# Kernel optimization log

Hardware: AMD Instinct MI355X
Metric: run time of the kernel (lower is better)

Reference implementation:

```python
import jax, jax.numpy as jnp
import numpy as np

N_USERS = 100000
N_ITEMS = 200000
N = N_USERS + N_ITEMS
E = 1200000
D = 64
HEADS = 4
GCN_LAYERS = 2


def setup_inputs() -> dict:
    key = jax.random.key(0)
    ks = jax.random.split(key, 10)
    s = 1.0 / np.sqrt(D)
    return {
        "uEmbeds": jax.random.normal(ks[0], (N_USERS, D), jnp.float32) * s,
        "iEmbeds": jax.random.normal(ks[1], (N_ITEMS, D), jnp.float32) * s,
        "qTrans": jax.random.normal(ks[2], (D, D), jnp.float32) * s,
        "kTrans": jax.random.normal(ks[3], (D, D), jnp.float32) * s,
        "vTrans": jax.random.normal(ks[4], (D, D), jnp.float32) * s,
        "enc_vals": jax.random.uniform(ks[5], (E,), jnp.float32),
        "enc_rows": jax.random.randint(ks[6], (E,), 0, N, jnp.int32),
        "enc_cols": jax.random.randint(ks[7], (E,), 0, N, jnp.int32),
        "dec_rows": jax.random.randint(ks[8], (E,), 0, N, jnp.int32),
        "dec_cols": jax.random.randint(ks[9], (E,), 0, N, jnp.int32),
    }


def _gcn(vals, rows, cols, embeds):
    # spmm: out[r] += vals[e] * embeds[cols[e]]
    msg = vals[:, None] * embeds[cols]  # [E, D]
    return jax.ops.segment_sum(msg, rows, num_segments=N)


def _gt(rows, cols, qT, kT, vT, embeds):
    dh = D // HEADS
    rowE = embeds[rows]  # [E, D]
    colE = embeds[cols]  # [E, D]
    q = (rowE @ qT).reshape(-1, HEADS, dh)
    k = (colE @ kT).reshape(-1, HEADS, dh)
    v = (colE @ vT).reshape(-1, HEADS, dh)
    att = jnp.clip(jnp.einsum('ehd,ehd->eh', q, k), -10.0, 10.0)
    expAtt = jnp.exp(att)  # [E, H]
    attNorm = jax.ops.segment_sum(expAtt, rows, num_segments=N)[rows]
    a = expAtt / (attNorm + 1e-8)
    res = (a[..., None] * v).reshape(-1, D)  # [E, D]
    return jax.ops.segment_sum(res, rows, num_segments=N)


def reference(uEmbeds, iEmbeds, qTrans, kTrans, vTrans,
              enc_vals, enc_rows, enc_cols, dec_rows, dec_cols):
    embeds = jnp.concatenate([uEmbeds, iEmbeds], axis=0)  # [N, D]
    embedsLst = [embeds]
    for _ in range(GCN_LAYERS):
        embedsLst.append(_gcn(enc_vals, enc_rows, enc_cols, embedsLst[-1]))
    embedsLst.append(_gt(dec_rows, dec_cols, qTrans, kTrans, vTrans, embedsLst[-1]))
    out = embedsLst[0]
    for e in embedsLst[1:]:
        out = out + e
    return out[:N_USERS], out[N_USERS:]
```

## Files before the change

kernel.cpp:

```cpp
#include <hip/hip_runtime.h>
#include <math.h>

#define N_USERS 100000
#define NTOT    300000
#define NEDGE   1200000
#define DIM     64

#define NPBS    256
#define BROWS2  1172
#define CAPS    5376
#define SCHUNK  4096
#define NCH     ((NEDGE + SCHUNK - 1) / SCHUNK)
#define PAD5    1280

typedef unsigned short ushort_t;
typedef unsigned int uint_t;
typedef __attribute__((ext_vector_type(8))) short short8;
typedef __attribute__((ext_vector_type(4))) float f32x4;

__device__ __forceinline__ float bf2f(ushort_t u) {
    return __uint_as_float(((uint_t)u) << 16);
}
__device__ __forceinline__ ushort_t f2bf(float x) {
    uint_t b = __float_as_uint(x);
    b += 0x7FFFu + ((b >> 16) & 1u);
    return (ushort_t)(b >> 16);
}


__global__ __launch_bounds__(256) void convert_emb0(
    const float* __restrict__ uE, const float* __restrict__ iE,
    ushort_t* __restrict__ emb0b) {
    int i = blockIdx.x * 256 + threadIdx.x;
    if (i >= NTOT * 16) return;
    float4 x = (i < N_USERS * 16) ? reinterpret_cast<const float4*>(uE)[i]
                                  : reinterpret_cast<const float4*>(iE)[i - N_USERS * 16];
    ushort4 o;
    o.x = f2bf(x.x); o.y = f2bf(x.y); o.z = f2bf(x.z); o.w = f2bf(x.w);
    reinterpret_cast<ushort4*>(emb0b)[i] = o;
}

__global__ void bt_prep(const float* __restrict__ qT, const float* __restrict__ kT,
                        const float* __restrict__ vT, ushort_t* __restrict__ Bt) {
    int t = threadIdx.x;
    for (int idx = t; idx < 4096; idx += 256) {
        int k = idx >> 6, c = idx & 63;
        Bt[c * 64 + k]        = f2bf(qT[idx]);
        Bt[4096 + c * 64 + k] = f2bf(kT[idx]);
        Bt[8192 + c * 64 + k] = f2bf(vT[idx]);
    }
}

__global__ void init_gcur(int* __restrict__ gE, int* __restrict__ gD) {
    int t = threadIdx.x;
    gE[t] = t * CAPS;
    gD[t] = t * CAPS;
}

__global__ __launch_bounds__(256) void bucket_stage(
    const int* __restrict__ enc_rows, const int* __restrict__ enc_cols,
    const float* __restrict__ enc_vals, const int* __restrict__ dec_rows,
    const int* __restrict__ dec_cols, int* __restrict__ gcurE,
    int* __restrict__ gcurD, int2* __restrict__ stE, int* __restrict__ stD) {
    __shared__ int cnt[NPBS];
    __shared__ int base[NPBS];
    __shared__ int run[NPBS];
    int t = threadIdx.x;
    bool enc = blockIdx.x < NCH;
    int cb = (enc ? blockIdx.x : blockIdx.x - NCH) * SCHUNK;
    int ce = min(cb + SCHUNK, NEDGE);
    const int* rows = enc ? enc_rows : dec_rows;
    cnt[t] = 0; run[t] = 0;
    __syncthreads();
    for (int i = cb + t; i < ce; i += 256) atomicAdd(&cnt[rows[i] / BROWS2], 1);
    __syncthreads();
    base[t] = atomicAdd(enc ? &gcurE[t] : &gcurD[t], cnt[t]);
    __syncthreads();
    if (enc) {
        for (int i = cb + t; i < ce; i += 256) {
            int r = rows[i];
            int p = r / BROWS2;
            int off = atomicAdd(&run[p], 1);
            int2 v;
            v.x = ((r - p * BROWS2) << 19) | enc_cols[i];
            v.y = __float_as_int(enc_vals[i]);
            stE[base[p] + off] = v;
        }
    } else {
        for (int i = cb + t; i < ce; i += 256) {
            int r = rows[i];
            int p = r / BROWS2;
            int off = atomicAdd(&run[p], 1);
            stD[base[p] + off] = ((r - p * BROWS2) << 19) | dec_cols[i];
        }
    }
}

__global__ __launch_bounds__(256) void scanB(
    const int* __restrict__ gcurE, const int* __restrict__ gcurD,
    int* __restrict__ bbE, int* __restrict__ bbD,
    int* __restrict__ rsE, int* __restrict__ rsD) {
    __shared__ int sh[256];
    int t = threadIdx.x;
    int c = gcurE[t] - t * CAPS;
    sh[t] = c; __syncthreads();
    for (int off = 1; off < 256; off <<= 1) {
        int x = (t >= off) ? sh[t - off] : 0; __syncthreads();
        sh[t] += x; __syncthreads();
    }
    bbE[t] = sh[t] - c;
    __syncthreads();
    int cd = gcurD[t] - t * CAPS;
    sh[t] = cd; __syncthreads();
    for (int off = 1; off < 256; off <<= 1) {
        int x = (t >= off) ? sh[t - off] : 0; __syncthreads();
        sh[t] += x; __syncthreads();
    }
    bbD[t] = sh[t] - cd;
    if (t == 0) { rsE[NTOT] = NEDGE; rsD[NTOT] = NEDGE; }
}

__global__ __launch_bounds__(256) void sort_b(
    const int* __restrict__ gcurE, const int* __restrict__ gcurD,
    const int* __restrict__ bbE, const int* __restrict__ bbD,
    const int2* __restrict__ stE, const int* __restrict__ stD,
    int2* __restrict__ penc, int* __restrict__ pdec,
    int* __restrict__ rsE, int* __restrict__ rsD) {
    __shared__ int cnt[PAD5];
    __shared__ int rowst[PAD5];
    __shared__ int tsum[256];
    __shared__ int2 outb[CAPS];
    int t = threadIdx.x;
    bool enc = blockIdx.x < NPBS;
    int b = enc ? blockIdx.x : blockIdx.x - NPBS;
    int rowbase = b * BROWS2;
    int s = b * CAPS;
    int e = enc ? gcurE[b] : gcurD[b];
    int gbase = enc ? bbE[b] : bbD[b];
    int n = e - s;

    for (int i = t; i < PAD5; i += 256) cnt[i] = 0;
    __syncthreads();
    if (enc) {
        for (int i = s + t; i < e; i += 256)
            atomicAdd(&cnt[((uint_t)stE[i].x) >> 19], 1);
    } else {
        for (int i = s + t; i < e; i += 256)
            atomicAdd(&cnt[((uint_t)stD[i]) >> 19], 1);
    }
    __syncthreads();
    int b5 = t * 5, sum = 0;
#pragma unroll
    for (int k = 0; k < 5; ++k) { int c = cnt[b5 + k]; rowst[b5 + k] = sum; sum += c; }
    tsum[t] = sum; __syncthreads();
    for (int off = 1; off < 256; off <<= 1) {
        int x = (t >= off) ? tsum[t - off] : 0; __syncthreads();
        tsum[t] += x; __syncthreads();
    }
    int excl = tsum[t] - sum;
#pragma unroll
    for (int k = 0; k < 5; ++k) {
        rowst[b5 + k] += excl;
        cnt[b5 + k] = rowst[b5 + k];
    }
    __syncthreads();

    if (enc) {
        for (int i = s + t; i < e; i += 256) {
            int2 v = stE[i];
            int lr = ((uint_t)v.x) >> 19;
            int pos = atomicAdd(&cnt[lr], 1);
            outb[pos] = make_int2(v.x & 0x7FFFF, v.y);
        }
        __syncthreads();
        for (int i = t; i < n; i += 256) penc[gbase + i] = outb[i];
        int nrows = min(BROWS2, NTOT - rowbase);
        for (int j = t; j < nrows; j += 256) rsE[rowbase + j] = gbase + rowst[j];
    } else {
        int* ob = (int*)outb;
        for (int i = s + t; i < e; i += 256) {
            int v = stD[i];
            int pos = atomicAdd(&cnt[((uint_t)v) >> 19], 1);
            ob[pos] = v & 0x7FFFF;
        }
        __syncthreads();
        for (int i = t; i < n; i += 256) pdec[gbase + i] = ob[i];
        int nrows = min(BROWS2, NTOT - rowbase);
        for (int j = t; j < nrows; j += 256) rsD[rowbase + j] = gbase + rowst[j];
    }
}

__global__ __launch_bounds__(256) void gcn_gather1(
    const int* __restrict__ rsE, const int2* __restrict__ penc,
    const ushort_t* __restrict__ emb0b, ushort_t* __restrict__ emb1b) {
    int t = blockIdx.x * 256 + threadIdx.x;
    int row = t >> 4, l = t & 15;
    if (row >= NTOT) return;
    int s = rsE[row], e = rsE[row + 1];
    float4 acc = {0.f, 0.f, 0.f, 0.f};
    for (int j = s; j < e; ++j) {
        int2 cv = penc[j];
        float v = __int_as_float(cv.y);
        ushort4 xb = reinterpret_cast<const ushort4*>(emb0b + (size_t)cv.x * DIM)[l];
        acc.x += v * bf2f(xb.x); acc.y += v * bf2f(xb.y);
        acc.z += v * bf2f(xb.z); acc.w += v * bf2f(xb.w);
    }
    ushort4 o;
    o.x = f2bf(acc.x); o.y = f2bf(acc.y); o.z = f2bf(acc.z); o.w = f2bf(acc.w);
    reinterpret_cast<ushort4*>(emb1b)[(size_t)row * 16 + l] = o;
}

__global__ __launch_bounds__(256) void gcn_gather2(
    const int* __restrict__ rsE, const int2* __restrict__ penc,
    const ushort_t* __restrict__ emb1b, const float* __restrict__ uE,
    const float* __restrict__ iE, ushort_t* __restrict__ emb2b,
    float* __restrict__ out) {
    int t = blockIdx.x * 256 + threadIdx.x;
    int row = t >> 4, l = t & 15;
    if (row >= NTOT) return;
    int s = rsE[row], e = rsE[row + 1];
    float4 acc = {0.f, 0.f, 0.f, 0.f};
    for (int j = s; j < e; ++j) {
        int2 cv = penc[j];
        float v = __int_as_float(cv.y);
        ushort4 xb = reinterpret_cast<const ushort4*>(emb1b + (size_t)cv.x * DIM)[l];
        acc.x += v * bf2f(xb.x); acc.y += v * bf2f(xb.y);
        acc.z += v * bf2f(xb.z); acc.w += v * bf2f(xb.w);
    }
    const float* e0p = (row < N_USERS) ? uE + (size_t)row * DIM
                                       : iE + (size_t)(row - N_USERS) * DIM;
    float4 e0 = reinterpret_cast<const float4*>(e0p)[l];
    ushort4 e1b = reinterpret_cast<const ushort4*>(emb1b)[(size_t)row * 16 + l];
    ushort4 o2;
    o2.x = f2bf(acc.x); o2.y = f2bf(acc.y); o2.z = f2bf(acc.z); o2.w = f2bf(acc.w);
    reinterpret_cast<ushort4*>(emb2b)[(size_t)row * 16 + l] = o2;
    float4 o;
    o.x = e0.x + bf2f(e1b.x) + acc.x; o.y = e0.y + bf2f(e1b.y) + acc.y;
    o.z = e0.z + bf2f(e1b.z) + acc.z; o.w = e0.w + bf2f(e1b.w) + acc.w;
    reinterpret_cast<float4*>(out)[(size_t)row * 16 + l] = o;
}

__global__ __launch_bounds__(256) void qkv_mfma(
    const ushort_t* __restrict__ emb2b, const ushort_t* __restrict__ Bt,
    float* __restrict__ Q, ushort_t* __restrict__ KV) {
    int tid = threadIdx.x;
    int w = tid >> 6, lane = tid & 63;
    int lr = lane & 15, lh = lane >> 4;
    int R0 = blockIdx.x * 256 + w * 64;

    short8 a[4][2];
    short8 z8 = {0, 0, 0, 0, 0, 0, 0, 0};
#pragma unroll
    for (int m = 0; m < 4; ++m) {
        int row = R0 + m * 16 + lr;
        if (row < NTOT) {
            const ushort_t* ap = emb2b + (size_t)row * 64 + lh * 8;
            a[m][0] = *reinterpret_cast<const short8*>(ap);
            a[m][1] = *reinterpret_cast<const short8*>(ap + 32);
        } else {
            a[m][0] = z8; a[m][1] = z8;
        }
    }

#pragma unroll
    for (int n = 0; n < 4; ++n) {
        int col = n * 16 + lr;
        const ushort_t* bp = Bt + (size_t)col * 64 + lh * 8;
        short8 bq0 = *reinterpret_cast<const short8*>(bp);
        short8 bq1 = *reinterpret_cast<const short8*>(bp + 32);
        short8 bk0 = *reinterpret_cast<const short8*>(bp + 4096);
        short8 bk1 = *reinterpret_cast<const short8*>(bp + 4096 + 32);
        short8 bv0 = *reinterpret_cast<const short8*>(bp + 8192);
        short8 bv1 = *reinterpret_cast<const short8*>(bp + 8192 + 32);
#pragma unroll
        for (int m = 0; m < 4; ++m) {
            f32x4 aq = {0.f, 0.f, 0.f, 0.f};
            f32x4 ak = {0.f, 0.f, 0.f, 0.f};
            f32x4 av = {0.f, 0.f, 0.f, 0.f};
            aq = __builtin_amdgcn_mfma_f32_16x16x32_bf16(a[m][0], bq0, aq, 0, 0, 0);
            aq = __builtin_amdgcn_mfma_f32_16x16x32_bf16(a[m][1], bq1, aq, 0, 0, 0);
            ak = __builtin_amdgcn_mfma_f32_16x16x32_bf16(a[m][0], bk0, ak, 0, 0, 0);
            ak = __builtin_amdgcn_mfma_f32_16x16x32_bf16(a[m][1], bk1, ak, 0, 0, 0);
            av = __builtin_amdgcn_mfma_f32_16x16x32_bf16(a[m][0], bv0, av, 0, 0, 0);
            av = __builtin_amdgcn_mfma_f32_16x16x32_bf16(a[m][1], bv1, av, 0, 0, 0);
            int rbase = R0 + m * 16 + lh * 4;
#pragma unroll
            for (int r = 0; r < 4; ++r) {
                int srow = rbase + r;
                if (srow < NTOT) {
                    Q[(size_t)srow * 64 + col] = aq[r];
                    KV[(size_t)srow * 128 + col] = f2bf(ak[r]);
                    KV[(size_t)srow * 128 + 64 + col] = f2bf(av[r]);
                }
            }
        }
    }
}

__global__ __launch_bounds__(256) void gt_fused(
    const int* __restrict__ rsD, const int* __restrict__ pdec,
    const float* __restrict__ Q, const ushort_t* __restrict__ KV,
    float* __restrict__ out) {
    int t = blockIdx.x * 256 + threadIdx.x;
    int row = t >> 4, l = t & 15;
    if (row >= NTOT) return;
    int s = rsD[row], e = rsD[row + 1];
    float4 q = reinterpret_cast<const float4*>(Q)[(size_t)row * 16 + l];
    float norm = 0.f;
    float4 acc = {0.f, 0.f, 0.f, 0.f};
    for (int j = s; j < e; ++j) {
        int c = pdec[j];
        const ushort_t* kvrow = KV + (size_t)c * 128;
        ushort4 kb = reinterpret_cast<const ushort4*>(kvrow)[l];
        ushort4 vb = reinterpret_cast<const ushort4*>(kvrow)[16 + l];
        float p = q.x * bf2f(kb.x) + q.y * bf2f(kb.y)
                + q.z * bf2f(kb.z) + q.w * bf2f(kb.w);
        p += __shfl_xor(p, 1);
        p += __shfl_xor(p, 2);
        p = fminf(10.f, fmaxf(-10.f, p));
        float ex = __expf(p);
        norm += ex;
        acc.x += ex * bf2f(vb.x); acc.y += ex * bf2f(vb.y);
        acc.z += ex * bf2f(vb.z); acc.w += ex * bf2f(vb.w);
    }
    float inv = 1.f / (norm + 1e-8f);
    float4 o = reinterpret_cast<float4*>(out)[(size_t)row * 16 + l];
    o.x += acc.x * inv; o.y += acc.y * inv;
    o.z += acc.z * inv; o.w += acc.w * inv;
    reinterpret_cast<float4*>(out)[(size_t)row * 16 + l] = o;
}

extern "C" void kernel_launch(void* const* d_in, const int* in_sizes, int n_in,
                              void* d_out, int out_size, void* d_ws, size_t ws_size,
                              hipStream_t stream) {
    const float* uE       = (const float*)d_in[0];
    const float* iE       = (const float*)d_in[1];
    const float* qT       = (const float*)d_in[2];
    const float* kT       = (const float*)d_in[3];
    const float* vT       = (const float*)d_in[4];
    const float* enc_vals = (const float*)d_in[5];
    const int*   enc_rows = (const int*)d_in[6];
    const int*   enc_cols = (const int*)d_in[7];
    const int*   dec_rows = (const int*)d_in[8];
    const int*   dec_cols = (const int*)d_in[9];
    float* out = (float*)d_out;

    const size_t ND = (size_t)NTOT * DIM;
    ushort_t* emb0b = (ushort_t*)d_ws;
    ushort_t* emb1b = emb0b + ND;
    ushort_t* emb2b = emb1b + ND;
    ushort_t* KV    = emb2b + ND;
    ushort_t* Bt    = KV + 2 * ND;
    int*      rsE   = (int*)(Bt + 3 * 4096);
    int*      rsD   = rsE + NTOT + 1;
    int2*     penc  = (int2*)(rsD + NTOT + 1);
    int*      pdec  = (int*)(penc + NEDGE);
    int*      gcurE = pdec + NEDGE;
    int*      gcurD = gcurE + NPBS;
    int*      bbE   = gcurD + NPBS;
    int*      bbD   = bbE + NPBS;

    float*    Q     = (float*)emb0b;
    int2*     stE   = (int2*)KV;
    int*      stD   = (int*)(stE + (size_t)NPBS * CAPS);

    const int GB  = (NTOT * 16) / 256;
    const int QB  = (NTOT + 255) / 256;

    init_gcur<<<1, 256, 0, stream>>>(gcurE, gcurD);
    convert_emb0<<<GB, 256, 0, stream>>>(uE, iE, emb0b);
    bt_prep<<<1, 256, 0, stream>>>(qT, kT, vT, Bt);

    bucket_stage<<<2 * NCH, 256, 0, stream>>>(enc_rows, enc_cols, enc_vals,
                                              dec_rows, dec_cols, gcurE, gcurD, stE, stD);
    scanB<<<1, 256, 0, stream>>>(gcurE, gcurD, bbE, bbD, rsE, rsD);
    sort_b<<<2 * NPBS, 256, 0, stream>>>(gcurE, gcurD, bbE, bbD, stE, stD,
                                         penc, pdec, rsE, rsD);

    gcn_gather1<<<GB, 256, 0, stream>>>(rsE, penc, emb0b, emb1b);
    gcn_gather2<<<GB, 256, 0, stream>>>(rsE, penc, emb1b, uE, iE, emb2b, out);

    qkv_mfma<<<QB, 256, 0, stream>>>(emb2b, Bt, Q, KV);
    gt_fused<<<GB, 256, 0, stream>>>(rsD, pdec, Q, KV, out);
}
```

Before: 409.7 us.

## Use one wavefront per row with 8 edge slots in gather kernels

The three CSR gather kernels (two GCN layers and the attention aggregation) now assign a full 64-lane wavefront to each row instead of 16 lanes. The lanes split into 8 edge slots of 8 lanes, each lane loading 16-byte chunks, so several edges per row are in flight at once. Partial sums are combined with cross-slot shuffle reductions and only slot 0 writes. This aims to raise memory-level parallelism for rows averaging about 4 edges. The cost is many idle slots on short rows, extra shuffle reductions, and four times as many threads launched.

```diff
diff --git a/kernel.cpp b/kernel.cpp
--- a/kernel.cpp
+++ b/kernel.cpp
@@ -16,6 +16,7 @@
 typedef unsigned short ushort_t;
 typedef unsigned int uint_t;
 typedef __attribute__((ext_vector_type(8))) short short8;
+typedef __attribute__((ext_vector_type(8))) unsigned short ushort8;
 typedef __attribute__((ext_vector_type(4))) float f32x4;
 
 __device__ __forceinline__ float bf2f(ushort_t u) {
@@ -193,21 +194,30 @@
 __global__ __launch_bounds__(256) void gcn_gather1(
     const int* __restrict__ rsE, const int2* __restrict__ penc,
     const ushort_t* __restrict__ emb0b, ushort_t* __restrict__ emb1b) {
-    int t = blockIdx.x * 256 + threadIdx.x;
-    int row = t >> 4, l = t & 15;
+    int tid = blockIdx.x * 256 + threadIdx.x;
+    int row = tid >> 6;
     if (row >= NTOT) return;
+    int lane = threadIdx.x & 63;
+    int slot = lane >> 3, sub = lane & 7;
     int s = rsE[row], e = rsE[row + 1];
-    float4 acc = {0.f, 0.f, 0.f, 0.f};
-    for (int j = s; j < e; ++j) {
+    float acc[8] = {};
+    for (int j = s + slot; j < e; j += 8) {
         int2 cv = penc[j];
         float v = __int_as_float(cv.y);
-        ushort4 xb = reinterpret_cast<const ushort4*>(emb0b + (size_t)cv.x * DIM)[l];
-        acc.x += v * bf2f(xb.x); acc.y += v * bf2f(xb.y);
-        acc.z += v * bf2f(xb.z); acc.w += v * bf2f(xb.w);
-    }
-    ushort4 o;
-    o.x = f2bf(acc.x); o.y = f2bf(acc.y); o.z = f2bf(acc.z); o.w = f2bf(acc.w);
-    reinterpret_cast<ushort4*>(emb1b)[(size_t)row * 16 + l] = o;
+        ushort8 xb = *reinterpret_cast<const ushort8*>(emb0b + (size_t)cv.x * DIM + sub * 8);
+#pragma unroll
+        for (int k = 0; k < 8; ++k) acc[k] += v * bf2f(xb[k]);
+    }
+#pragma unroll
+    for (int m = 8; m <= 32; m <<= 1)
+#pragma unroll
+        for (int k = 0; k < 8; ++k) acc[k] += __shfl_xor(acc[k], m);
+    if (slot == 0) {
+        ushort8 o;
+#pragma unroll
+        for (int k = 0; k < 8; ++k) o[k] = f2bf(acc[k]);
+        *reinterpret_cast<ushort8*>(emb1b + (size_t)row * DIM + sub * 8) = o;
+    }
 }
 
 __global__ __launch_bounds__(256) void gcn_gather2(
@@ -215,29 +225,42 @@
     const ushort_t* __restrict__ emb1b, const float* __restrict__ uE,
     const float* __restrict__ iE, ushort_t* __restrict__ emb2b,
     float* __restrict__ out) {
-    int t = blockIdx.x * 256 + threadIdx.x;
-    int row = t >> 4, l = t & 15;
+    int tid = blockIdx.x * 256 + threadIdx.x;
+    int row = tid >> 6;
     if (row >= NTOT) return;
+    int lane = threadIdx.x & 63;
+    int slot = lane >> 3, sub = lane & 7;
     int s = rsE[row], e = rsE[row + 1];
-    float4 acc = {0.f, 0.f, 0.f, 0.f};
-    for (int j = s; j < e; ++j) {
+    float acc[8] = {};
+    for (int j = s + slot; j < e; j += 8) {
         int2 cv = penc[j];
         float v = __int_as_float(cv.y);
-        ushort4 xb = reinterpret_cast<const ushort4*>(emb1b + (size_t)cv.x * DIM)[l];
-        acc.x += v * bf2f(xb.x); acc.y += v * bf2f(xb.y);
-        acc.z += v * bf2f(xb.z); acc.w += v * bf2f(xb.w);
-    }
-    const float* e0p = (row < N_USERS) ? uE + (size_t)row * DIM
-                                       : iE + (size_t)(row - N_USERS) * DIM;
-    float4 e0 = reinterpret_cast<const float4*>(e0p)[l];
-    ushort4 e1b = reinterpret_cast<const ushort4*>(emb1b)[(size_t)row * 16 + l];
-    ushort4 o2;
-    o2.x = f2bf(acc.x); o2.y = f2bf(acc.y); o2.z = f2bf(acc.z); o2.w = f2bf(acc.w);
-    reinterpret_cast<ushort4*>(emb2b)[(size_t)row * 16 + l] = o2;
-    float4 o;
-    o.x = e0.x + bf2f(e1b.x) + acc.x; o.y = e0.y + bf2f(e1b.y) + acc.y;
-    o.z = e0.z + bf2f(e1b.z) + acc.z; o.w = e0.w + bf2f(e1b.w) + acc.w;
-    reinterpret_cast<float4*>(out)[(size_t)row * 16 + l] = o;
+        ushort8 xb = *reinterpret_cast<const ushort8*>(emb1b + (size_t)cv.x * DIM + sub * 8);
+#pragma unroll
+        for (int k = 0; k < 8; ++k) acc[k] += v * bf2f(xb[k]);
+    }
+#pragma unroll
+    for (int m = 8; m <= 32; m <<= 1)
+#pragma unroll
+        for (int k = 0; k < 8; ++k) acc[k] += __shfl_xor(acc[k], m);
+    if (slot == 0) {
+        ushort8 o2;
+#pragma unroll
+        for (int k = 0; k < 8; ++k) o2[k] = f2bf(acc[k]);
+        *reinterpret_cast<ushort8*>(emb2b + (size_t)row * DIM + sub * 8) = o2;
+        const float* e0p = (row < N_USERS) ? uE + (size_t)row * DIM
+                                           : iE + (size_t)(row - N_USERS) * DIM;
+        float4 e0a = reinterpret_cast<const float4*>(e0p)[sub * 2];
+        float4 e0b = reinterpret_cast<const float4*>(e0p)[sub * 2 + 1];
+        ushort8 e1 = *reinterpret_cast<const ushort8*>(emb1b + (size_t)row * DIM + sub * 8);
+        float4 oa, ob;
+        oa.x = e0a.x + bf2f(e1[0]) + acc[0]; oa.y = e0a.y + bf2f(e1[1]) + acc[1];
+        oa.z = e0a.z + bf2f(e1[2]) + acc[2]; oa.w = e0a.w + bf2f(e1[3]) + acc[3];
+        ob.x = e0b.x + bf2f(e1[4]) + acc[4]; ob.y = e0b.y + bf2f(e1[5]) + acc[5];
+        ob.z = e0b.z + bf2f(e1[6]) + acc[6]; ob.w = e0b.w + bf2f(e1[7]) + acc[7];
+        reinterpret_cast<float4*>(out + (size_t)row * DIM)[sub * 2] = oa;
+        reinterpret_cast<float4*>(out + (size_t)row * DIM)[sub * 2 + 1] = ob;
+    }
 }
 
 __global__ __launch_bounds__(256) void qkv_mfma(
@@ -301,33 +324,53 @@
     const int* __restrict__ rsD, const int* __restrict__ pdec,
     const float* __restrict__ Q, const ushort_t* __restrict__ KV,
     float* __restrict__ out) {
-    int t = blockIdx.x * 256 + threadIdx.x;
-    int row = t >> 4, l = t & 15;
+    int tid = blockIdx.x * 256 + threadIdx.x;
+    int row = tid >> 6;
     if (row >= NTOT) return;
+    int lane = threadIdx.x & 63;
+    int slot = lane >> 3, sub = lane & 7;
     int s = rsD[row], e = rsD[row + 1];
-    float4 q = reinterpret_cast<const float4*>(Q)[(size_t)row * 16 + l];
+    float qv[8];
+    {
+        float4 qa = reinterpret_cast<const float4*>(Q + (size_t)row * DIM)[sub * 2];
+        float4 qb = reinterpret_cast<const float4*>(Q + (size_t)row * DIM)[sub * 2 + 1];
+        qv[0] = qa.x; qv[1] = qa.y; qv[2] = qa.z; qv[3] = qa.w;
+        qv[4] = qb.x; qv[5] = qb.y; qv[6] = qb.z; qv[7] = qb.w;
+    }
     float norm = 0.f;
-    float4 acc = {0.f, 0.f, 0.f, 0.f};
-    for (int j = s; j < e; ++j) {
+    float acc[8] = {};
+    for (int j = s + slot; j < e; j += 8) {
         int c = pdec[j];
         const ushort_t* kvrow = KV + (size_t)c * 128;
-        ushort4 kb = reinterpret_cast<const ushort4*>(kvrow)[l];
-        ushort4 vb = reinterpret_cast<const ushort4*>(kvrow)[16 + l];
-        float p = q.x * bf2f(kb.x) + q.y * bf2f(kb.y)
-                + q.z * bf2f(kb.z) + q.w * bf2f(kb.w);
+        ushort8 kb = *reinterpret_cast<const ushort8*>(kvrow + sub * 8);
+        ushort8 vb = *reinterpret_cast<const ushort8*>(kvrow + 64 + sub * 8);
+        float p = 0.f;
+#pragma unroll
+        for (int k = 0; k < 8; ++k) p += qv[k] * bf2f(kb[k]);
         p += __shfl_xor(p, 1);
-        p += __shfl_xor(p, 2);
         p = fminf(10.f, fmaxf(-10.f, p));
         float ex = __expf(p);
         norm += ex;
-        acc.x += ex * bf2f(vb.x); acc.y += ex * bf2f(vb.y);
-        acc.z += ex * bf2f(vb.z); acc.w += ex * bf2f(vb.w);
-    }
-    float inv = 1.f / (norm + 1e-8f);
-    float4 o = reinterpret_cast<float4*>(out)[(size_t)row * 16 + l];
-    o.x += acc.x * inv; o.y += acc.y * inv;
-    o.z += acc.z * inv; o.w += acc.w * inv;
-    reinterpret_cast<float4*>(out)[(size_t)row * 16 + l] = o;
+#pragma unroll
+        for (int k = 0; k < 8; ++k) acc[k] += ex * bf2f(vb[k]);
+    }
+#pragma unroll
+    for (int m = 8; m <= 32; m <<= 1) {
+        norm += __shfl_xor(norm, m);
+#pragma unroll
+        for (int k = 0; k < 8; ++k) acc[k] += __shfl_xor(acc[k], m);
+    }
+    if (slot == 0) {
+        float inv = 1.f / (norm + 1e-8f);
+        float4 oa = reinterpret_cast<float4*>(out + (size_t)row * DIM)[sub * 2];
+        float4 ob = reinterpret_cast<float4*>(out + (size_t)row * DIM)[sub * 2 + 1];
+        oa.x += acc[0] * inv; oa.y += acc[1] * inv;
+        oa.z += acc[2] * inv; oa.w += acc[3] * inv;
+        ob.x += acc[4] * inv; ob.y += acc[5] * inv;
+        ob.z += acc[6] * inv; ob.w += acc[7] * inv;
+        reinterpret_cast<float4*>(out + (size_t)row * DIM)[sub * 2] = oa;
+        reinterpret_cast<float4*>(out + (size_t)row * DIM)[sub * 2 + 1] = ob;
+    }
 }
 
 extern "C" void kernel_launch(void* const* d_in, const int* in_sizes, int n_in,
@@ -365,6 +408,7 @@
     int*      stD   = (int*)(stE + (size_t)NPBS * CAPS);
 
     const int GB  = (NTOT * 16) / 256;
+    const int WB  = (NTOT * 64 + 255) / 256;
     const int QB  = (NTOT + 255) / 256;
 
     init_gcur<<<1, 256, 0, stream>>>(gcurE, gcurD);
@@ -377,9 +421,9 @@
     sort_b<<<2 * NPBS, 256, 0, stream>>>(gcurE, gcurD, bbE, bbD, stE, stD,
                                          penc, pdec, rsE, rsD);
 
-    gcn_gather1<<<GB, 256, 0, stream>>>(rsE, penc, emb0b, emb1b);
-    gcn_gather2<<<GB, 256, 0, stream>>>(rsE, penc, emb1b, uE, iE, emb2b, out);
+    gcn_gather1<<<WB, 256, 0, stream>>>(rsE, penc, emb0b, emb1b);
+    gcn_gather2<<<WB, 256, 0, stream>>>(rsE, penc, emb1b, uE, iE, emb2b, out);
 
     qkv_mfma<<<QB, 256, 0, stream>>>(emb2b, Bt, Q, KV);
-    gt_fused<<<GB, 256, 0, stream>>>(rsD, pdec, Q, KV, out);
-}
+    gt_fused<<<WB, 256, 0, stream>>>(rsD, pdec, Q, KV, out);
+}
```

Result: slower. 492.9 us (+20.3%).

## Split each row's edges across two half-groups and interleave K/V layout

Applied to the files above, without the earlier changes.

The three gather kernels now give each row 32 threads in two 16-lane slots. Each slot processes alternate edges, and the two partial sums are combined with a cross-half shuffle. This adds memory-level parallelism for rows with several edges, at the cost of twice the threads and idle lanes on low-degree rows. The qkv kernel also writes K and V interleaved per 4-column group, so the attention kernel fetches both with a single 16-byte load instead of two 8-byte loads.

```diff
diff --git a/kernel.cpp b/kernel.cpp
--- a/kernel.cpp
+++ b/kernel.cpp
@@ -16,6 +16,7 @@
 typedef unsigned short ushort_t;
 typedef unsigned int uint_t;
 typedef __attribute__((ext_vector_type(8))) short short8;
+typedef __attribute__((ext_vector_type(8))) unsigned short ushort8;
 typedef __attribute__((ext_vector_type(4))) float f32x4;
 
 __device__ __forceinline__ float bf2f(ushort_t u) {
@@ -193,21 +194,27 @@
 __global__ __launch_bounds__(256) void gcn_gather1(
     const int* __restrict__ rsE, const int2* __restrict__ penc,
     const ushort_t* __restrict__ emb0b, ushort_t* __restrict__ emb1b) {
-    int t = blockIdx.x * 256 + threadIdx.x;
-    int row = t >> 4, l = t & 15;
+    int tid = blockIdx.x * 256 + threadIdx.x;
+    int row = tid >> 5;
     if (row >= NTOT) return;
+    int lane = threadIdx.x & 31;
+    int slot = lane >> 4, l = lane & 15;
     int s = rsE[row], e = rsE[row + 1];
     float4 acc = {0.f, 0.f, 0.f, 0.f};
-    for (int j = s; j < e; ++j) {
+    for (int j = s + slot; j < e; j += 2) {
         int2 cv = penc[j];
         float v = __int_as_float(cv.y);
         ushort4 xb = reinterpret_cast<const ushort4*>(emb0b + (size_t)cv.x * DIM)[l];
         acc.x += v * bf2f(xb.x); acc.y += v * bf2f(xb.y);
         acc.z += v * bf2f(xb.z); acc.w += v * bf2f(xb.w);
     }
-    ushort4 o;
-    o.x = f2bf(acc.x); o.y = f2bf(acc.y); o.z = f2bf(acc.z); o.w = f2bf(acc.w);
-    reinterpret_cast<ushort4*>(emb1b)[(size_t)row * 16 + l] = o;
+    acc.x += __shfl_xor(acc.x, 16); acc.y += __shfl_xor(acc.y, 16);
+    acc.z += __shfl_xor(acc.z, 16); acc.w += __shfl_xor(acc.w, 16);
+    if (slot == 0) {
+        ushort4 o;
+        o.x = f2bf(acc.x); o.y = f2bf(acc.y); o.z = f2bf(acc.z); o.w = f2bf(acc.w);
+        reinterpret_cast<ushort4*>(emb1b)[(size_t)row * 16 + l] = o;
+    }
 }
 
 __global__ __launch_bounds__(256) void gcn_gather2(
@@ -215,29 +222,35 @@
     const ushort_t* __restrict__ emb1b, const float* __restrict__ uE,
     const float* __restrict__ iE, ushort_t* __restrict__ emb2b,
     float* __restrict__ out) {
-    int t = blockIdx.x * 256 + threadIdx.x;
-    int row = t >> 4, l = t & 15;
+    int tid = blockIdx.x * 256 + threadIdx.x;
+    int row = tid >> 5;
     if (row >= NTOT) return;
+    int lane = threadIdx.x & 31;
+    int slot = lane >> 4, l = lane & 15;
     int s = rsE[row], e = rsE[row + 1];
     float4 acc = {0.f, 0.f, 0.f, 0.f};
-    for (int j = s; j < e; ++j) {
+    for (int j = s + slot; j < e; j += 2) {
         int2 cv = penc[j];
         float v = __int_as_float(cv.y);
         ushort4 xb = reinterpret_cast<const ushort4*>(emb1b + (size_t)cv.x * DIM)[l];
         acc.x += v * bf2f(xb.x); acc.y += v * bf2f(xb.y);
         acc.z += v * bf2f(xb.z); acc.w += v * bf2f(xb.w);
     }
-    const float* e0p = (row < N_USERS) ? uE + (size_t)row * DIM
-                                       : iE + (size_t)(row - N_USERS) * DIM;
-    float4 e0 = reinterpret_cast<const float4*>(e0p)[l];
-    ushort4 e1b = reinterpret_cast<const ushort4*>(emb1b)[(size_t)row * 16 + l];
-    ushort4 o2;
-    o2.x = f2bf(acc.x); o2.y = f2bf(acc.y); o2.z = f2bf(acc.z); o2.w = f2bf(acc.w);
-    reinterpret_cast<ushort4*>(emb2b)[(size_t)row * 16 + l] = o2;
-    float4 o;
-    o.x = e0.x + bf2f(e1b.x) + acc.x; o.y = e0.y + bf2f(e1b.y) + acc.y;
-    o.z = e0.z + bf2f(e1b.z) + acc.z; o.w = e0.w + bf2f(e1b.w) + acc.w;
-    reinterpret_cast<float4*>(out)[(size_t)row * 16 + l] = o;
+    acc.x += __shfl_xor(acc.x, 16); acc.y += __shfl_xor(acc.y, 16);
+    acc.z += __shfl_xor(acc.z, 16); acc.w += __shfl_xor(acc.w, 16);
+    if (slot == 0) {
+        ushort4 o2;
+        o2.x = f2bf(acc.x); o2.y = f2bf(acc.y); o2.z = f2bf(acc.z); o2.w = f2bf(acc.w);
+        reinterpret_cast<ushort4*>(emb2b)[(size_t)row * 16 + l] = o2;
+        const float* e0p = (row < N_USERS) ? uE + (size_t)row * DIM
+                                           : iE + (size_t)(row - N_USERS) * DIM;
+        float4 e0 = reinterpret_cast<const float4*>(e0p)[l];
+        ushort4 e1 = reinterpret_cast<const ushort4*>(emb1b)[(size_t)row * 16 + l];
+        float4 o;
+        o.x = e0.x + bf2f(e1.x) + acc.x; o.y = e0.y + bf2f(e1.y) + acc.y;
+        o.z = e0.z + bf2f(e1.z) + acc.z; o.w = e0.w + bf2f(e1.w) + acc.w;
+        reinterpret_cast<float4*>(out)[(size_t)row * 16 + l] = o;
+    }
 }
 
 __global__ __launch_bounds__(256) void qkv_mfma(
@@ -272,6 +285,7 @@
         short8 bk1 = *reinterpret_cast<const short8*>(bp + 4096 + 32);
         short8 bv0 = *reinterpret_cast<const short8*>(bp + 8192);
         short8 bv1 = *reinterpret_cast<const short8*>(bp + 8192 + 32);
+        int ip = ((col >> 2) << 3) + (col & 3);
 #pragma unroll
         for (int m = 0; m < 4; ++m) {
             f32x4 aq = {0.f, 0.f, 0.f, 0.f};
@@ -289,8 +303,8 @@
                 int srow = rbase + r;
                 if (srow < NTOT) {
                     Q[(size_t)srow * 64 + col] = aq[r];
-                    KV[(size_t)srow * 128 + col] = f2bf(ak[r]);
-                    KV[(size_t)srow * 128 + 64 + col] = f2bf(av[r]);
+                    KV[(size_t)srow * 128 + ip] = f2bf(ak[r]);
+                    KV[(size_t)srow * 128 + ip + 4] = f2bf(av[r]);
                 }
             }
         }
@@ -301,33 +315,38 @@
     const int* __restrict__ rsD, const int* __restrict__ pdec,
     const float* __restrict__ Q, const ushort_t* __restrict__ KV,
     float* __restrict__ out) {
-    int t = blockIdx.x * 256 + threadIdx.x;
-    int row = t >> 4, l = t & 15;
+    int tid = blockIdx.x * 256 + threadIdx.x;
+    int row = tid >> 5;
     if (row >= NTOT) return;
+    int lane = threadIdx.x & 31;
+    int slot = lane >> 4, l = lane & 15;
     int s = rsD[row], e = rsD[row + 1];
     float4 q = reinterpret_cast<const float4*>(Q)[(size_t)row * 16 + l];
     float norm = 0.f;
     float4 acc = {0.f, 0.f, 0.f, 0.f};
-    for (int j = s; j < e; ++j) {
+    for (int j = s + slot; j < e; j += 2) {
         int c = pdec[j];
-        const ushort_t* kvrow = KV + (size_t)c * 128;
-        ushort4 kb = reinterpret_cast<const ushort4*>(kvrow)[l];
-        ushort4 vb = reinterpret_cast<const ushort4*>(kvrow)[16 + l];
-        float p = q.x * bf2f(kb.x) + q.y * bf2f(kb.y)
-                + q.z * bf2f(kb.z) + q.w * bf2f(kb.w);
+        ushort8 kv = *reinterpret_cast<const ushort8*>(KV + (size_t)c * 128 + l * 8);
+        float p = q.x * bf2f(kv[0]) + q.y * bf2f(kv[1])
+                + q.z * bf2f(kv[2]) + q.w * bf2f(kv[3]);
         p += __shfl_xor(p, 1);
         p += __shfl_xor(p, 2);
         p = fminf(10.f, fmaxf(-10.f, p));
         float ex = __expf(p);
         norm += ex;
-        acc.x += ex * bf2f(vb.x); acc.y += ex * bf2f(vb.y);
-        acc.z += ex * bf2f(vb.z); acc.w += ex * bf2f(vb.w);
-    }
-    float inv = 1.f / (norm + 1e-8f);
-    float4 o = reinterpret_cast<float4*>(out)[(size_t)row * 16 + l];
-    o.x += acc.x * inv; o.y += acc.y * inv;
-    o.z += acc.z * inv; o.w += acc.w * inv;
-    reinterpret_cast<float4*>(out)[(size_t)row * 16 + l] = o;
+        acc.x += ex * bf2f(kv[4]); acc.y += ex * bf2f(kv[5]);
+        acc.z += ex * bf2f(kv[6]); acc.w += ex * bf2f(kv[7]);
+    }
+    norm  += __shfl_xor(norm, 16);
+    acc.x += __shfl_xor(acc.x, 16); acc.y += __shfl_xor(acc.y, 16);
+    acc.z += __shfl_xor(acc.z, 16); acc.w += __shfl_xor(acc.w, 16);
+    if (slot == 0) {
+        float inv = 1.f / (norm + 1e-8f);
+        float4 o = reinterpret_cast<float4*>(out)[(size_t)row * 16 + l];
+        o.x += acc.x * inv; o.y += acc.y * inv;
+        o.z += acc.z * inv; o.w += acc.w * inv;
+        reinterpret_cast<float4*>(out)[(size_t)row * 16 + l] = o;
+    }
 }
 
 extern "C" void kernel_launch(void* const* d_in, const int* in_sizes, int n_in,
@@ -365,6 +384,7 @@
     int*      stD   = (int*)(stE + (size_t)NPBS * CAPS);
 
     const int GB  = (NTOT * 16) / 256;
+    const int WB2 = (NTOT * 32 + 255) / 256;
     const int QB  = (NTOT + 255) / 256;
 
     init_gcur<<<1, 256, 0, stream>>>(gcurE, gcurD);
@@ -377,9 +397,9 @@
     sort_b<<<2 * NPBS, 256, 0, stream>>>(gcurE, gcurD, bbE, bbD, stE, stD,
                                          penc, pdec, rsE, rsD);
 
-    gcn_gather1<<<GB, 256, 0, stream>>>(rsE, penc, emb0b, emb1b);
-    gcn_gather2<<<GB, 256, 0, stream>>>(rsE, penc, emb1b, uE, iE, emb2b, out);
+    gcn_gather1<<<WB2, 256, 0, stream>>>(rsE, penc, emb0b, emb1b);
+    gcn_gather2<<<WB2, 256, 0, stream>>>(rsE, penc, emb1b, uE, iE, emb2b, out);
 
     qkv_mfma<<<QB, 256, 0, stream>>>(emb2b, Bt, Q, KV);
-    gt_fused<<<GB, 256, 0, stream>>>(rsD, pdec, Q, KV, out);
-}
+    gt_fused<<<WB2, 256, 0, stream>>>(rsD, pdec, Q, KV, out);
+}
```

After: 408.2 us. Within noise of the previous version (-0.4%).
